# Kernel tuning notes

Measured on AMD Instinct MI355X. Metric: run time of the kernel, lower is better.

Reference implementation:

```python
import jax, jax.numpy as jnp
import numpy as np

V, E, H = 50000, 200, 128
B, R, S, W = 16, 10, 20, 64


def gru_last(x, lengths, Wih, Whh, bih, bhh, reverse=False):
    # x: [N,T,D], lengths: [N] -> final valid hidden state [N,H]
    # Masked-update scan: h only updates on valid timesteps, so after the full
    # scan h equals the packed-sequence final hidden (fwd: t=len-1; bwd: t=0).
    N, T, _ = x.shape
    Hd = Whh.shape[1]
    xi = x @ Wih.T + bih                      # [N,T,3H] input gates, precomputed
    t = jnp.arange(T)
    if reverse:
        xi = xi[:, ::-1]
        valid = (T - 1 - t)[None, :] < lengths[:, None]
    else:
        valid = t[None, :] < lengths[:, None]

    def step(h, inp):
        xg, v = inp
        hg = h @ Whh.T + bhh
        r = jax.nn.sigmoid(xg[:, :Hd] + hg[:, :Hd])
        z = jax.nn.sigmoid(xg[:, Hd:2 * Hd] + hg[:, Hd:2 * Hd])
        n = jnp.tanh(xg[:, 2 * Hd:] + r * hg[:, 2 * Hd:])
        hn = (1.0 - z) * n + z * h
        return jnp.where(v[:, None], hn, h), None

    h0 = jnp.zeros((N, Hd), x.dtype)
    hT, _ = jax.lax.scan(step, h0, (jnp.swapaxes(xi, 0, 1), valid.T))
    return hT


def bigru_last(x, lengths, pf, pb):
    hf = gru_last(x, lengths, *pf, reverse=False)
    hb = gru_last(x, lengths, *pb, reverse=True)
    return 0.5 * (hf + hb)  # reduce bidirectional h_n to hid_dim (mean of dirs)


def setup_inputs() -> dict:
    key = jax.random.key(0)
    ks = jax.random.split(key, 24)

    def gn(k, shape, s=0.1):
        return jax.random.normal(k, shape, dtype=jnp.float32) * s

    return {
        "inputs": jax.random.randint(ks[0], (B, R, S, W), 0, V),
        "sent_lengths": jax.random.randint(ks[1], (B, R, S), 1, W + 1),
        "sent_counts": jax.random.randint(ks[2], (B, R), 1, S + 1),
        "embed": gn(ks[3], (V, E), 1.0),
        "wWih_f": gn(ks[4], (3 * H, E)), "wWhh_f": gn(ks[5], (3 * H, H)),
        "wbih_f": gn(ks[6], (3 * H,)), "wbhh_f": gn(ks[7], (3 * H,)),
        "wWih_b": gn(ks[8], (3 * H, E)), "wWhh_b": gn(ks[9], (3 * H, H)),
        "wbih_b": gn(ks[10], (3 * H,)), "wbhh_b": gn(ks[11], (3 * H,)),
        "sWih_f": gn(ks[12], (3 * H, H)), "sWhh_f": gn(ks[13], (3 * H, H)),
        "sbih_f": gn(ks[14], (3 * H,)), "sbhh_f": gn(ks[15], (3 * H,)),
        "sWih_b": gn(ks[16], (3 * H, H)), "sWhh_b": gn(ks[17], (3 * H, H)),
        "sbih_b": gn(ks[18], (3 * H,)), "sbhh_b": gn(ks[19], (3 * H,)),
        "fc1_w": gn(ks[20], (H // 2, H)), "fc1_b": gn(ks[21], (H // 2,)),
        "fc2_w": gn(ks[22], (1, H // 2)), "fc2_b": gn(ks[23], (1,)),
    }


def reference(inputs, sent_lengths, sent_counts, embed,
              wWih_f, wWhh_f, wbih_f, wbhh_f, wWih_b, wWhh_b, wbih_b, wbhh_b,
              sWih_f, sWhh_f, sbih_f, sbhh_f, sWih_b, sWhh_b, sbih_b, sbhh_b,
              fc1_w, fc1_b, fc2_w, fc2_b):
    b, r, s, w = inputs.shape
    emb = embed[inputs]                                   # [B,R,S,W,E]
    x = emb.reshape(b * r * s, w, -1)
    wlens = sent_lengths.reshape(-1)
    # Word-level BiGRU over all sentences at once (flattened ragged batch)
    sent_rep = bigru_last(x, wlens,
                          (wWih_f, wWhh_f, wbih_f, wbhh_f),
                          (wWih_b, wWhh_b, wbih_b, wbhh_b))  # [B*R*S, H]
    xs = sent_rep.reshape(b * r, s, -1)
    slens = sent_counts.reshape(-1)
    # Sentence-level BiGRU over all reviews at once
    rev = bigru_last(xs, slens,
                     (sWih_f, sWhh_f, sbih_f, sbhh_f),
                     (sWih_b, sWhh_b, sbih_b, sbhh_b)).reshape(b, r, -1)
    h = jax.nn.selu(rev @ fc1_w.T + fc1_b)                # [B,R,H//2]
    r_stars = (h @ fc2_w.T + fc2_b)[..., 0]               # [B,R]
    p_stars = r_stars.mean(-1)                            # [B]
    return p_stars, r_stars
```

## Files before the change

kernel.cpp:

```cpp
#include <hip/hip_runtime.h>
#include <hip/hip_bf16.h>
#include <cstddef>

#define VOCAB 50000
#define EDIM  200
#define HDIM  128
#define BB 16
#define RR 10
#define SS 20
#define WW 64
#define NSENT (BB*RR*SS)
#define NREV  (BB*RR)
#define G3    (3*HDIM)
#define NPROJ (2*G3)

static __device__ __forceinline__ short f2bf(float f) {
    union { float f; unsigned u; } v; v.f = f;
    unsigned r = v.u + 0x7FFFu + ((v.u >> 16) & 1u);
    return (short)(r >> 16);
}
static __device__ __forceinline__ short f2bf_t(float f) {
    union { float f; unsigned u; } v; v.f = f;
    return (short)(v.u >> 16);
}
static __device__ __forceinline__ float bf2f(short s) {
    union { unsigned u; float f; } v;
    v.u = ((unsigned)(unsigned short)s) << 16;
    return v.f;
}
static __device__ __forceinline__ float frcp(float x) {
    return __builtin_amdgcn_rcpf(x);
}
static __device__ __forceinline__ float fsigmoid(float x) {
    return frcp(1.f + __expf(-x));
}
static __device__ __forceinline__ float ftanh(float x) {
    float y = __expf(-2.f * fabsf(x));
    float t = (1.f - y) * frcp(1.f + y);
    return copysignf(t, x);
}

#define GM_LDK 40

template<int KREAL, int KPAD, bool AVG>
__global__ __launch_bounds__(256, 2) void gemm_mfma_bias(
    const float* __restrict__ A0, const float* __restrict__ A1, int M,
    const float* __restrict__ B0, const float* __restrict__ B1,
    const float* __restrict__ bias0, const float* __restrict__ bias1,
    float* __restrict__ C)
{
    using bf16x8 = __attribute__((ext_vector_type(8))) short;
    using f32x4  = __attribute__((ext_vector_type(4))) float;

    const int ct = blockIdx.x;
    const int rt = blockIdx.y;
    const int tid = threadIdx.x;
    const int lane = tid & 63;
    const int wid  = tid >> 6;
    const int rlane = lane & 15;
    const int kgrp  = lane >> 4;

    const int rowBase = rt * 128;
    const int colBase = ct * 128;
    const float* Bsrc = (colBase < G3) ? B0 : B1;
    const int bcol = (colBase < G3) ? colBase : (colBase - G3);

    __shared__ short Ahi[128][GM_LDK], Alo[128][GM_LDK];
    __shared__ short Bhi[128][GM_LDK], Blo[128][GM_LDK];

    const int wrow = (wid >> 1) * 64;
    const int wcol = (wid & 1) * 64;

    f32x4 acc[4][4];
    #pragma unroll
    for (int i = 0; i < 4; ++i)
        #pragma unroll
        for (int j = 0; j < 4; ++j) acc[i][j] = {0.f, 0.f, 0.f, 0.f};

    const int srow = tid >> 1;
    const int skh  = (tid & 1) << 4;

    for (int k0 = 0; k0 < KPAD; k0 += 32) {
        {
            const int grow = rowBase + srow;
            float v[16];
            #pragma unroll
            for (int i = 0; i < 4; ++i) {
                const int k = k0 + skh + i * 4;
                float4 x = {0.f, 0.f, 0.f, 0.f};
                if (grow < M && k + 3 < KREAL) {
                    x = *(const float4*)&A0[(size_t)grow * KREAL + k];
                    if (AVG) {
                        float4 y = *(const float4*)&A1[(size_t)grow * KREAL + k];
                        x.x = 0.5f * (x.x + y.x); x.y = 0.5f * (x.y + y.y);
                        x.z = 0.5f * (x.z + y.z); x.w = 0.5f * (x.w + y.w);
                    }
                }
                v[4*i+0] = x.x; v[4*i+1] = x.y; v[4*i+2] = x.z; v[4*i+3] = x.w;
            }
            bf16x8 h0, h1, l0, l1;
            #pragma unroll
            for (int i = 0; i < 8; ++i) {
                short a = f2bf_t(v[i]);
                h0[i] = a; l0[i] = f2bf(v[i] - bf2f(a));
                short b = f2bf_t(v[i + 8]);
                h1[i] = b; l1[i] = f2bf(v[i + 8] - bf2f(b));
            }
            *(bf16x8*)&Ahi[srow][skh]     = h0;
            *(bf16x8*)&Ahi[srow][skh + 8] = h1;
            *(bf16x8*)&Alo[srow][skh]     = l0;
            *(bf16x8*)&Alo[srow][skh + 8] = l1;
        }
        {
            const int gcol = bcol + srow;
            float v[16];
            #pragma unroll
            for (int i = 0; i < 4; ++i) {
                const int k = k0 + skh + i * 4;
                float4 x = {0.f, 0.f, 0.f, 0.f};
                if (k + 3 < KREAL)
                    x = *(const float4*)&Bsrc[(size_t)gcol * KREAL + k];
                v[4*i+0] = x.x; v[4*i+1] = x.y; v[4*i+2] = x.z; v[4*i+3] = x.w;
            }
            bf16x8 h0, h1, l0, l1;
            #pragma unroll
            for (int i = 0; i < 8; ++i) {
                short a = f2bf_t(v[i]);
                h0[i] = a; l0[i] = f2bf(v[i] - bf2f(a));
                short b = f2bf_t(v[i + 8]);
                h1[i] = b; l1[i] = f2bf(v[i + 8] - bf2f(b));
            }
            *(bf16x8*)&Bhi[srow][skh]     = h0;
            *(bf16x8*)&Bhi[srow][skh + 8] = h1;
            *(bf16x8*)&Blo[srow][skh]     = l0;
            *(bf16x8*)&Blo[srow][skh + 8] = l1;
        }
        __syncthreads();
        bf16x8 ah[4], al[4], bh[4], bl[4];
        #pragma unroll
        for (int mr = 0; mr < 4; ++mr) {
            ah[mr] = *(const bf16x8*)&Ahi[wrow + mr * 16 + rlane][kgrp * 8];
            al[mr] = *(const bf16x8*)&Alo[wrow + mr * 16 + rlane][kgrp * 8];
        }
        #pragma unroll
        for (int nc = 0; nc < 4; ++nc) {
            bh[nc] = *(const bf16x8*)&Bhi[wcol + nc * 16 + rlane][kgrp * 8];
            bl[nc] = *(const bf16x8*)&Blo[wcol + nc * 16 + rlane][kgrp * 8];
        }
        #pragma unroll
        for (int mr = 0; mr < 4; ++mr)
            #pragma unroll
            for (int nc = 0; nc < 4; ++nc) {
                acc[mr][nc] = __builtin_amdgcn_mfma_f32_16x16x32_bf16(
                    ah[mr], bh[nc], acc[mr][nc], 0, 0, 0);
                acc[mr][nc] = __builtin_amdgcn_mfma_f32_16x16x32_bf16(
                    ah[mr], bl[nc], acc[mr][nc], 0, 0, 0);
                acc[mr][nc] = __builtin_amdgcn_mfma_f32_16x16x32_bf16(
                    al[mr], bh[nc], acc[mr][nc], 0, 0, 0);
            }
        __syncthreads();
    }

    const float* bs = (colBase < G3) ? bias0 : bias1;
    #pragma unroll
    for (int nc = 0; nc < 4; ++nc) {
        const int c = wcol + nc * 16 + rlane;
        const float bv = bs[bcol + c];
        #pragma unroll
        for (int mr = 0; mr < 4; ++mr) {
            #pragma unroll
            for (int r = 0; r < 4; ++r) {
                const int grow = rowBase + wrow + mr * 16 + kgrp * 4 + r;
                if (grow < M)
                    C[(size_t)grow * NPROJ + colBase + c] = acc[mr][nc][r] + bv;
            }
        }
    }
}

__global__ __launch_bounds__(256) void sort_all(
    const int* __restrict__ len1, int* __restrict__ order1,
    const int* __restrict__ len2, int* __restrict__ order2)
{
    __shared__ int hist[65];
    const int tid = threadIdx.x;

    for (int i = tid; i < 65; i += 256) hist[i] = 0;
    __syncthreads();
    for (int i = tid; i < NSENT; i += 256) atomicAdd(&hist[len1[i]], 1);
    __syncthreads();
    if (tid == 0) {
        int acc = 0;
        for (int l = 1; l <= WW; ++l) { int c = hist[l]; hist[l] = acc; acc += c; }
    }
    __syncthreads();
    for (int i = tid; i < NSENT; i += 256) {
        int pos = atomicAdd(&hist[len1[i]], 1);
        order1[pos] = i;
    }
    __syncthreads();
    for (int i = tid; i < 65; i += 256) hist[i] = 0;
    __syncthreads();
    for (int i = tid; i < NREV; i += 256) atomicAdd(&hist[len2[i]], 1);
    __syncthreads();
    if (tid == 0) {
        int acc = 0;
        for (int l = 1; l <= SS; ++l) { int c = hist[l]; hist[l] = acc; acc += c; }
    }
    __syncthreads();
    for (int i = tid; i < NREV; i += 256) {
        int pos = atomicAdd(&hist[len2[i]], 1);
        order2[pos] = i;
    }
}

template<bool WORD, int TMAX>
__global__ __launch_bounds__(512, 2) void gru_mfma(
    const float* __restrict__ table,
    const int*   __restrict__ tokens,
    const int*   __restrict__ lengths,
    const int*   __restrict__ order,
    const float* __restrict__ Whh_f, const float* __restrict__ Whh_b,
    const float* __restrict__ bhh_f, const float* __restrict__ bhh_b,
    float* __restrict__ hout_f, float* __restrict__ hout_b,
    int numSeq, int numTiles)
{
    using bf16x8 = __attribute__((ext_vector_type(8))) short;
    using f32x4  = __attribute__((ext_vector_type(4))) float;

    const int dir  = (blockIdx.x >= numTiles) ? 1 : 0;
    const int rawt = dir ? (blockIdx.x - numTiles) : blockIdx.x;
    const int tile = numTiles - 1 - rawt;
    const int base = tile * 16;
    const int tid  = threadIdx.x;
    const int lane = tid & 63;
    const int wid  = tid >> 6;
    const int rlane = lane & 15;
    const int kgrp  = lane >> 4;
    const int e = wid * 16 + rlane;

    __shared__ __align__(16) short sh_hi[2][16][136];
    __shared__ __align__(16) short sh_lo[2][16][136];
    __shared__ int sh_len[16];
    __shared__ int sh_ord[16];
    __shared__ int sh_tok[WORD ? 16 * WW : 1];
    __shared__ int sh_maxlen;

    const float* Whh = dir ? Whh_b : Whh_f;
    const float* bhh = dir ? bhh_b : bhh_f;
    bf16x8 Bhi[3][4], Blo[3][4];
    float bb[3];
    #pragma unroll
    for (int nt = 0; nt < 3; ++nt) {
        const int cb = nt * HDIM + wid * 16;
        const float* wrow = Whh + (size_t)(cb + rlane) * HDIM;
        bb[nt] = bhh[cb + rlane];
        #pragma unroll
        for (int kc = 0; kc < 4; ++kc) {
            const float* wp = wrow + kc * 32 + kgrp * 8;
            float4 w0 = *(const float4*)wp;
            float4 w1 = *(const float4*)(wp + 4);
            float wv[8] = {w0.x, w0.y, w0.z, w0.w, w1.x, w1.y, w1.z, w1.w};
            #pragma unroll
            for (int j = 0; j < 8; ++j) {
                short hi = f2bf_t(wv[j]);
                Bhi[nt][kc][j] = hi;
                Blo[nt][kc][j] = f2bf(wv[j] - bf2f(hi));
            }
        }
    }

    if (tid < 16) {
        int pos = base + tid;
        int seq = (pos < numSeq) ? order[pos] : -1;
        sh_ord[tid] = seq;
        sh_len[tid] = (seq >= 0) ? lengths[seq] : 0;
    }
    __syncthreads();
    if (WORD) {
        for (int f = tid; f < 16 * WW; f += 512) {
            int s = f >> 6;
            int seq = sh_ord[s];
            sh_tok[f] = (seq >= 0) ? tokens[(size_t)seq * WW + (f & 63)] : 0;
        }
    }
    for (int u = tid; u < 2 * 16 * 136; u += 512) {
        ((short*)sh_hi)[u] = 0;
        ((short*)sh_lo)[u] = 0;
    }
    if (tid == 0) {
        int m = 0;
        for (int s = 0; s < 16; ++s) m = max(m, sh_len[s]);
        sh_maxlen = m;
    }
    int lens[4], ords[4];
    #pragma unroll
    for (int j = 0; j < 4; ++j) {
        lens[j] = sh_len[4 * kgrp + j];
        ords[j] = sh_ord[4 * kgrp + j];
    }
    __syncthreads();
    const int maxlen = sh_maxlen;

    auto fetch_xg = [&](int t, float* fr, float* fz, float* fn) {
        #pragma unroll
        for (int j = 0; j < 4; ++j) {
            fr[j] = 0.f; fz[j] = 0.f; fn[j] = 0.f;
            if (t < lens[j]) {
                int tt = dir ? (lens[j] - 1 - t) : t;
                size_t row;
                if (WORD) row = (size_t)sh_tok[(4 * kgrp + j) * WW + tt];
                else      row = (size_t)ords[j] * TMAX + tt;
                const float* xg = table + row * NPROJ + dir * G3 + e;
                fr[j] = xg[0]; fz[j] = xg[HDIM]; fn[j] = xg[2 * HDIM];
            }
        }
    };

    float hold[4] = {0.f, 0.f, 0.f, 0.f};
    float pAr[4], pAz[4], pAn[4];
    float pBr[4], pBz[4], pBn[4];
    fetch_xg(0, pAr, pAz, pAn);
    fetch_xg(1, pBr, pBz, pBn);

#define GRU_STEP(T, PR, PZ, PN)                                               \
    {                                                                         \
        const int cur = (T) & 1, nxt = cur ^ 1;                               \
        bf16x8 ah[4], al[4];                                                  \
        _Pragma("unroll")                                                     \
        for (int kc = 0; kc < 4; ++kc) {                                      \
            ah[kc] = *(const bf16x8*)&sh_hi[cur][rlane][kc * 32 + kgrp * 8];  \
            al[kc] = *(const bf16x8*)&sh_lo[cur][rlane][kc * 32 + kgrp * 8];  \
        }                                                                     \
        f32x4 acc[3];                                                         \
        _Pragma("unroll")                                                     \
        for (int nt = 0; nt < 3; ++nt) {                                      \
            acc[nt] = {0.f, 0.f, 0.f, 0.f};                                   \
            _Pragma("unroll")                                                 \
            for (int kc = 0; kc < 4; ++kc)                                    \
                acc[nt] = __builtin_amdgcn_mfma_f32_16x16x32_bf16(            \
                    ah[kc], Bhi[nt][kc], acc[nt], 0, 0, 0);                   \
            _Pragma("unroll")                                                 \
            for (int kc = 0; kc < 4; ++kc)                                    \
                acc[nt] = __builtin_amdgcn_mfma_f32_16x16x32_bf16(            \
                    ah[kc], Blo[nt][kc], acc[nt], 0, 0, 0);                   \
            _Pragma("unroll")                                                 \
            for (int kc = 0; kc < 4; ++kc)                                    \
                acc[nt] = __builtin_amdgcn_mfma_f32_16x16x32_bf16(            \
                    al[kc], Bhi[nt][kc], acc[nt], 0, 0, 0);                   \
        }                                                                     \
        _Pragma("unroll")                                                     \
        for (int j = 0; j < 4; ++j) {                                         \
            if ((T) < lens[j]) {                                              \
                float hgr = acc[0][j] + bb[0];                                \
                float hgz = acc[1][j] + bb[1];                                \
                float hgn = acc[2][j] + bb[2];                                \
                float rg = fsigmoid(PR[j] + hgr);                             \
                float zg = fsigmoid(PZ[j] + hgz);                             \
                float ng = ftanh(PN[j] + rg * hgn);                           \
                hold[j] = (1.f - zg) * ng + zg * hold[j];                     \
            }                                                                 \
        }                                                                     \
        fetch_xg((T) + 2, PR, PZ, PN);                                        \
        _Pragma("unroll")                                                     \
        for (int j = 0; j < 4; ++j) {                                         \
            const int s = 4 * kgrp + j;                                       \
            short hi = f2bf_t(hold[j]);                                       \
            sh_hi[nxt][s][e] = hi;                                            \
            sh_lo[nxt][s][e] = f2bf(hold[j] - bf2f(hi));                      \
        }                                                                     \
        __syncthreads();                                                      \
    }

    int t = 0;
    for (; t + 1 < maxlen; t += 2) {
        GRU_STEP(t,     pAr, pAz, pAn);
        GRU_STEP(t + 1, pBr, pBz, pBn);
    }
    if (t < maxlen) {
        GRU_STEP(t, pAr, pAz, pAn);
    }
#undef GRU_STEP

    float* hout = dir ? hout_b : hout_f;
    #pragma unroll
    for (int j = 0; j < 4; ++j) {
        if (ords[j] >= 0)
            hout[(size_t)ords[j] * HDIM + e] = hold[j];
    }
}

__global__ __launch_bounds__(64) void head_kernel(
    const float* __restrict__ hsf, const float* __restrict__ hsb,
    const float* __restrict__ fc1_w, const float* __restrict__ fc1_b,
    const float* __restrict__ fc2_w, const float* __restrict__ fc2_b,
    float* __restrict__ out)
{
    const int br = blockIdx.x;
    const int j = threadIdx.x;
    __shared__ float rev[HDIM];
    for (int ee = j; ee < HDIM; ee += 64)
        rev[ee] = 0.5f * (hsf[(size_t)br * HDIM + ee] + hsb[(size_t)br * HDIM + ee]);
    __syncthreads();
    float acc = 0.f;
    #pragma unroll
    for (int k = 0; k < HDIM; ++k)
        acc = fmaf(fc1_w[(size_t)j * HDIM + k], rev[k], acc);
    acc += fc1_b[j];
    const float alpha = 1.6732632423543772f;
    const float scale = 1.0507009873554805f;
    float h1 = scale * (acc > 0.f ? acc : alpha * (expf(acc) - 1.f));
    float contrib = h1 * fc2_w[j];
    #pragma unroll
    for (int off = 32; off > 0; off >>= 1)
        contrib += __shfl_down(contrib, off);
    if (j == 0) out[16 + br] = contrib + fc2_b[0];
}

__global__ void mean_kernel(float* __restrict__ out)
{
    int b = threadIdx.x;
    if (b < BB) {
        float s = 0.f;
        for (int r = 0; r < RR; ++r) s += out[16 + b * RR + r];
        out[b] = s / (float)RR;
    }
}

extern "C" void kernel_launch(void* const* d_in, const int* in_sizes, int n_in,
                              void* d_out, int out_size, void* d_ws, size_t ws_size,
                              hipStream_t stream)
{
    const int*   inputs       = (const int*)d_in[0];
    const int*   sent_lengths = (const int*)d_in[1];
    const int*   sent_counts  = (const int*)d_in[2];
    const float* embed   = (const float*)d_in[3];
    const float* wWih_f  = (const float*)d_in[4];
    const float* wWhh_f  = (const float*)d_in[5];
    const float* wbih_f  = (const float*)d_in[6];
    const float* wbhh_f  = (const float*)d_in[7];
    const float* wWih_b  = (const float*)d_in[8];
    const float* wWhh_b  = (const float*)d_in[9];
    const float* wbih_b  = (const float*)d_in[10];
    const float* wbhh_b  = (const float*)d_in[11];
    const float* sWih_f  = (const float*)d_in[12];
    const float* sWhh_f  = (const float*)d_in[13];
    const float* sbih_f  = (const float*)d_in[14];
    const float* sbhh_f  = (const float*)d_in[15];
    const float* sWih_b  = (const float*)d_in[16];
    const float* sWhh_b  = (const float*)d_in[17];
    const float* sbih_b  = (const float*)d_in[18];
    const float* sbhh_b  = (const float*)d_in[19];
    const float* fc1_w   = (const float*)d_in[20];
    const float* fc1_b   = (const float*)d_in[21];
    const float* fc2_w   = (const float*)d_in[22];
    const float* fc2_b   = (const float*)d_in[23];

    float* ws = (float*)d_ws;
    const size_t projT_elems = (size_t)VOCAB * NPROJ;
    const size_t xgs_elems   = (size_t)NSENT * NPROJ;
    const size_t h_elems     = (size_t)NSENT * HDIM;
    const size_t hs_elems    = (size_t)NREV * HDIM;
    float* projT = ws;
    float* xgs   = projT + projT_elems;
    float* hf    = xgs + xgs_elems;
    float* hb    = hf + h_elems;
    float* hsf   = hb + h_elems;
    float* hsb   = hsf + hs_elems;
    int* order1 = (int*)(hsb + hs_elems);
    int* order2 = order1 + NSENT;

    size_t need = (projT_elems + xgs_elems + 2*h_elems + 2*hs_elems) * sizeof(float)
                + (NSENT + NREV) * sizeof(int);
    if (ws_size < need) return;

    sort_all<<<1, 256, 0, stream>>>(sent_lengths, order1, sent_counts, order2);

    {
        dim3 grid(NPROJ / 128, (VOCAB + 127) / 128);
        gemm_mfma_bias<EDIM, 224, false><<<grid, 256, 0, stream>>>(
            embed, nullptr, VOCAB,
            wWih_f, wWih_b, wbih_f, wbih_b, projT);
    }
    {
        int numTiles = NSENT / 16;
        gru_mfma<true, WW><<<2 * numTiles, 512, 0, stream>>>(
            projT, inputs, sent_lengths, order1,
            wWhh_f, wWhh_b, wbhh_f, wbhh_b,
            hf, hb, NSENT, numTiles);
    }
    {
        dim3 grid(NPROJ / 128, (NSENT + 127) / 128);
        gemm_mfma_bias<HDIM, HDIM, true><<<grid, 256, 0, stream>>>(
            hf, hb, NSENT,
            sWih_f, sWih_b, sbih_f, sbih_b, xgs);
    }
    {
        int numTiles = NREV / 16;
        gru_mfma<false, SS><<<2 * numTiles, 512, 0, stream>>>(
            xgs, nullptr, sent_counts, order2,
            sWhh_f, sWhh_b, sbhh_f, sbhh_b,
            hsf, hsb, NREV, numTiles);
    }
    head_kernel<<<NREV, 64, 0, stream>>>(hsf, hsb, fc1_w, fc1_b, fc2_w, fc2_b,
                                         (float*)d_out);
    mean_kernel<<<1, 64, 0, stream>>>((float*)d_out);
}
```

Before: 275.2 us.

## Pre-split GEMM weights to bf16 hi/lo and register-prefetch next K tile

Adds a preconv kernel that converts the input-projection weight matrices into bf16 hi/lo halves, padded to the K tile, once per call. The GEMM then loads these directly instead of re-splitting the weights in every block. The GEMM also loads the next K slice of A and B into registers before running the MFMA work on the current slice, so global loads overlap with compute. The cost is four extra small kernel launches, more workspace, and higher register pressure from the prefetch buffers.

Result: slower. 299.1 us (+8.7%).

```diff
diff --git a/kernel.cpp b/kernel.cpp
--- a/kernel.cpp
+++ b/kernel.cpp
@@ -40,18 +40,49 @@
     return copysignf(t, x);
 }
 
+using bf16x8 = __attribute__((ext_vector_type(8))) short;
+using f32x4  = __attribute__((ext_vector_type(4))) float;
+
+template<int KREAL, int KPAD>
+__global__ __launch_bounds__(256) void preconv(
+    const float* __restrict__ A0, int Mreal,
+    short* __restrict__ hi, short* __restrict__ lo, int ngroups)
+{
+    int g = blockIdx.x * 256 + threadIdx.x;
+    if (g >= ngroups) return;
+    int row = g / (KPAD / 8);
+    int k   = (g % (KPAD / 8)) * 8;
+    float v[8];
+    if (row < Mreal && k < KREAL) {
+        const float* p = A0 + (size_t)row * KREAL + k;
+        float4 a = *(const float4*)p;
+        float4 b = *(const float4*)(p + 4);
+        v[0]=a.x; v[1]=a.y; v[2]=a.z; v[3]=a.w;
+        v[4]=b.x; v[5]=b.y; v[6]=b.z; v[7]=b.w;
+    } else {
+        #pragma unroll
+        for (int j = 0; j < 8; ++j) v[j] = 0.f;
+    }
+    bf16x8 h, l;
+    #pragma unroll
+    for (int j = 0; j < 8; ++j) {
+        short t = f2bf_t(v[j]);
+        h[j] = t;
+        l[j] = f2bf(v[j] - bf2f(t));
+    }
+    *(bf16x8*)&hi[(size_t)row * KPAD + k] = h;
+    *(bf16x8*)&lo[(size_t)row * KPAD + k] = l;
+}
+
 #define GM_LDK 40
 
 template<int KREAL, int KPAD, bool AVG>
-__global__ __launch_bounds__(256, 2) void gemm_mfma_bias(
+__global__ __launch_bounds__(256, 2) void gemm_v4(
     const float* __restrict__ A0, const float* __restrict__ A1, int M,
-    const float* __restrict__ B0, const float* __restrict__ B1,
+    const short* __restrict__ Bhi_g, const short* __restrict__ Blo_g,
     const float* __restrict__ bias0, const float* __restrict__ bias1,
     float* __restrict__ C)
 {
-    using bf16x8 = __attribute__((ext_vector_type(8))) short;
-    using f32x4  = __attribute__((ext_vector_type(4))) float;
-
     const int ct = blockIdx.x;
     const int rt = blockIdx.y;
     const int tid = threadIdx.x;
@@ -62,8 +93,6 @@
 
     const int rowBase = rt * 128;
     const int colBase = ct * 128;
-    const float* Bsrc = (colBase < G3) ? B0 : B1;
-    const int bcol = (colBase < G3) ? colBase : (colBase - G3);
 
     __shared__ short Ahi[128][GM_LDK], Alo[128][GM_LDK];
     __shared__ short Bhi[128][GM_LDK], Blo[128][GM_LDK];
@@ -79,25 +108,44 @@
 
     const int srow = tid >> 1;
     const int skh  = (tid & 1) << 4;
+    const int grow = rowBase + srow;
+    const size_t brow = (size_t)(colBase + srow) * KPAD;
+
+    float4 va[4];
+    bf16x8 vbh0, vbh1, vbl0, vbl1;
+
+    auto loadA = [&](int k0) {
+        #pragma unroll
+        for (int i = 0; i < 4; ++i) {
+            const int k = k0 + skh + i * 4;
+            float4 x = {0.f, 0.f, 0.f, 0.f};
+            if (grow < M && k + 3 < KREAL) {
+                x = *(const float4*)&A0[(size_t)grow * KREAL + k];
+                if (AVG) {
+                    float4 y = *(const float4*)&A1[(size_t)grow * KREAL + k];
+                    x.x = 0.5f * (x.x + y.x); x.y = 0.5f * (x.y + y.y);
+                    x.z = 0.5f * (x.z + y.z); x.w = 0.5f * (x.w + y.w);
+                }
+            }
+            va[i] = x;
+        }
+    };
+    auto loadB = [&](int k0) {
+        vbh0 = *(const bf16x8*)&Bhi_g[brow + k0 + skh];
+        vbh1 = *(const bf16x8*)&Bhi_g[brow + k0 + skh + 8];
+        vbl0 = *(const bf16x8*)&Blo_g[brow + k0 + skh];
+        vbl1 = *(const bf16x8*)&Blo_g[brow + k0 + skh + 8];
+    };
+
+    loadA(0);
+    loadB(0);
 
     for (int k0 = 0; k0 < KPAD; k0 += 32) {
         {
-            const int grow = rowBase + srow;
-            float v[16];
-            #pragma unroll
-            for (int i = 0; i < 4; ++i) {
-                const int k = k0 + skh + i * 4;
-                float4 x = {0.f, 0.f, 0.f, 0.f};
-                if (grow < M && k + 3 < KREAL) {
-                    x = *(const float4*)&A0[(size_t)grow * KREAL + k];
-                    if (AVG) {
-                        float4 y = *(const float4*)&A1[(size_t)grow * KREAL + k];
-                        x.x = 0.5f * (x.x + y.x); x.y = 0.5f * (x.y + y.y);
-                        x.z = 0.5f * (x.z + y.z); x.w = 0.5f * (x.w + y.w);
-                    }
-                }
-                v[4*i+0] = x.x; v[4*i+1] = x.y; v[4*i+2] = x.z; v[4*i+3] = x.w;
-            }
+            float v[16] = {va[0].x, va[0].y, va[0].z, va[0].w,
+                           va[1].x, va[1].y, va[1].z, va[1].w,
+                           va[2].x, va[2].y, va[2].z, va[2].w,
+                           va[3].x, va[3].y, va[3].z, va[3].w};
             bf16x8 h0, h1, l0, l1;
             #pragma unroll
             for (int i = 0; i < 8; ++i) {
@@ -110,32 +158,16 @@
             *(bf16x8*)&Ahi[srow][skh + 8] = h1;
             *(bf16x8*)&Alo[srow][skh]     = l0;
             *(bf16x8*)&Alo[srow][skh + 8] = l1;
-        }
-        {
-            const int gcol = bcol + srow;
-            float v[16];
-            #pragma unroll
-            for (int i = 0; i < 4; ++i) {
-                const int k = k0 + skh + i * 4;
-                float4 x = {0.f, 0.f, 0.f, 0.f};
-                if (k + 3 < KREAL)
-                    x = *(const float4*)&Bsrc[(size_t)gcol * KREAL + k];
-                v[4*i+0] = x.x; v[4*i+1] = x.y; v[4*i+2] = x.z; v[4*i+3] = x.w;
-            }
-            bf16x8 h0, h1, l0, l1;
-            #pragma unroll
-            for (int i = 0; i < 8; ++i) {
-                short a = f2bf_t(v[i]);
-                h0[i] = a; l0[i] = f2bf(v[i] - bf2f(a));
-                short b = f2bf_t(v[i + 8]);
-                h1[i] = b; l1[i] = f2bf(v[i + 8] - bf2f(b));
-            }
-            *(bf16x8*)&Bhi[srow][skh]     = h0;
-            *(bf16x8*)&Bhi[srow][skh + 8] = h1;
-            *(bf16x8*)&Blo[srow][skh]     = l0;
-            *(bf16x8*)&Blo[srow][skh + 8] = l1;
+            *(bf16x8*)&Bhi[srow][skh]     = vbh0;
+            *(bf16x8*)&Bhi[srow][skh + 8] = vbh1;
+            *(bf16x8*)&Blo[srow][skh]     = vbl0;
+            *(bf16x8*)&Blo[srow][skh + 8] = vbl1;
         }
         __syncthreads();
+        if (k0 + 32 < KPAD) {
+            loadA(k0 + 32);
+            loadB(k0 + 32);
+        }
         bf16x8 ah[4], al[4], bh[4], bl[4];
         #pragma unroll
         for (int mr = 0; mr < 4; ++mr) {
@@ -162,6 +194,7 @@
     }
 
     const float* bs = (colBase < G3) ? bias0 : bias1;
+    const int bcol = (colBase < G3) ? colBase : (colBase - G3);
     #pragma unroll
     for (int nc = 0; nc < 4; ++nc) {
         const int c = wcol + nc * 16 + rlane;
@@ -170,9 +203,9 @@
         for (int mr = 0; mr < 4; ++mr) {
             #pragma unroll
             for (int r = 0; r < 4; ++r) {
-                const int grow = rowBase + wrow + mr * 16 + kgrp * 4 + r;
-                if (grow < M)
-                    C[(size_t)grow * NPROJ + colBase + c] = acc[mr][nc][r] + bv;
+                const int grow2 = rowBase + wrow + mr * 16 + kgrp * 4 + r;
+                if (grow2 < M)
+                    C[(size_t)grow2 * NPROJ + colBase + c] = acc[mr][nc][r] + bv;
             }
         }
     }
@@ -225,9 +258,6 @@
     float* __restrict__ hout_f, float* __restrict__ hout_b,
     int numSeq, int numTiles)
 {
-    using bf16x8 = __attribute__((ext_vector_type(8))) short;
-    using f32x4  = __attribute__((ext_vector_type(4))) float;
-
     const int dir  = (blockIdx.x >= numTiles) ? 1 : 0;
     const int rawt = dir ? (blockIdx.x - numTiles) : blockIdx.x;
     const int tile = numTiles - 1 - rawt;
@@ -467,20 +497,38 @@
     float* hb    = hf + h_elems;
     float* hsf   = hb + h_elems;
     float* hsb   = hsf + hs_elems;
-    int* order1 = (int*)(hsb + hs_elems);
-    int* order2 = order1 + NSENT;
+    int* order1  = (int*)(hsb + hs_elems);
+    int* order2  = order1 + NSENT;
+    short* Bw_hi = (short*)(order2 + NREV);
+    short* Bw_lo = Bw_hi + 768 * 224;
+    short* Sw_hi = Bw_lo + 768 * 224;
+    short* Sw_lo = Sw_hi + 768 * 128;
 
     size_t need = (projT_elems + xgs_elems + 2*h_elems + 2*hs_elems) * sizeof(float)
-                + (NSENT + NREV) * sizeof(int);
+                + (NSENT + NREV) * sizeof(int)
+                + (size_t)(2 * 768 * 224 + 2 * 768 * 128) * sizeof(short);
     if (ws_size < need) return;
 
     sort_all<<<1, 256, 0, stream>>>(sent_lengths, order1, sent_counts, order2);
+    {
+        int ng = 384 * 224 / 8;
+        preconv<EDIM, 224><<<(ng + 255) / 256, 256, 0, stream>>>(
+            wWih_f, 384, Bw_hi, Bw_lo, ng);
+        preconv<EDIM, 224><<<(ng + 255) / 256, 256, 0, stream>>>(
+            wWih_b, 384, Bw_hi + 384 * 224, Bw_lo + 384 * 224, ng);
+    }
+    {
+        int ng = 384 * 128 / 8;
+        preconv<HDIM, HDIM><<<(ng + 255) / 256, 256, 0, stream>>>(
+            sWih_f, 384, Sw_hi, Sw_lo, ng);
+        preconv<HDIM, HDIM><<<(ng + 255) / 256, 256, 0, stream>>>(
+            sWih_b, 384, Sw_hi + 384 * 128, Sw_lo + 384 * 128, ng);
+    }
 
     {
         dim3 grid(NPROJ / 128, (VOCAB + 127) / 128);
-        gemm_mfma_bias<EDIM, 224, false><<<grid, 256, 0, stream>>>(
-            embed, nullptr, VOCAB,
-            wWih_f, wWih_b, wbih_f, wbih_b, projT);
+        gemm_v4<EDIM, 224, false><<<grid, 256, 0, stream>>>(
+            embed, nullptr, VOCAB, Bw_hi, Bw_lo, wbih_f, wbih_b, projT);
     }
     {
         int numTiles = NSENT / 16;
@@ -491,9 +539,8 @@
     }
     {
         dim3 grid(NPROJ / 128, (NSENT + 127) / 128);
-        gemm_mfma_bias<HDIM, HDIM, true><<<grid, 256, 0, stream>>>(
-            hf, hb, NSENT,
-            sWih_f, sWih_b, sbih_f, sbih_b, xgs);
+        gemm_v4<HDIM, HDIM, true><<<grid, 256, 0, stream>>>(
+            hf, hb, NSENT, Sw_hi, Sw_lo, sbih_f, sbih_b, xgs);
     }
     {
         int numTiles = NREV / 16;
```
